# Performance work log

Hardware: AMD Instinct MI355X
Metric: run time of the kernel (lower is better)

The kernel has to match this reference:

```python
import jax, jax.numpy as jnp
import numpy as np

N = 100000      # nodes
E = 1600000     # edges (avg degree 16)
NFEAT = 128
NHID = 128
LRELU_SLOPE = 0.2

def setup_inputs() -> dict:
    key = jax.random.key(0)
    ks = jax.random.split(key, 12)
    s = 1.0 / np.sqrt(NFEAT)
    inp = {}
    inp["x"] = jax.random.normal(ks[0], (N, NFEAT), dtype=jnp.float32)
    inp["edge_row"] = jax.random.randint(ks[1], (E,), 0, N, dtype=jnp.int32)
    inp["edge_col"] = jax.random.randint(ks[2], (E,), 0, N, dtype=jnp.int32)
    inp["edge_val"] = jax.random.uniform(ks[3], (E,), dtype=jnp.float32)
    inp["norm"] = jax.random.uniform(ks[4], (N, 1), dtype=jnp.float32) * 16.0 + 1.0
    # Relation params (bias-free Linears, torch layout y = x @ W.T)
    inp["Wg1"] = jax.random.uniform(ks[5], (NFEAT, NFEAT), minval=-s, maxval=s, dtype=jnp.float32)
    inp["Wg2"] = jax.random.uniform(ks[6], (NFEAT, NFEAT), minval=-s, maxval=s, dtype=jnp.float32)
    inp["Wb1"] = jax.random.uniform(ks[7], (NFEAT, NFEAT), minval=-s, maxval=s, dtype=jnp.float32)
    inp["Wb2"] = jax.random.uniform(ks[8], (NFEAT, NFEAT), minval=-s, maxval=s, dtype=jnp.float32)
    inp["r"] = jax.random.uniform(ks[9], (1, NFEAT), minval=-s, maxval=s, dtype=jnp.float32)
    # GraphConv weight [nfeat, nhid]
    inp["gc_w"] = jax.random.uniform(ks[10], (NFEAT, NHID), minval=-s, maxval=s, dtype=jnp.float32)
    return inp

def _spmm(edge_row, edge_col, edge_val, h):
    # sparse [N,N] @ dense [N,D] via gather + segment-sum
    return jax.ops.segment_sum(edge_val[:, None] * h[edge_col], edge_row, num_segments=N)

def reference(x, edge_row, edge_col, edge_val, norm, Wg1, Wg2, Wb1, Wb2, r, gc_w):
    # neighbor = sp.mm(adj, x)
    neighbor = _spmm(edge_row, edge_col, edge_val, x)
    # Relation (ver=1, ablation=0): FiLM-modulated transE relation vector
    gamma = jax.nn.leaky_relu(x @ Wg1.T + neighbor @ Wg2.T, LRELU_SLOPE) + 1.0
    beta = jax.nn.leaky_relu(x @ Wb1.T + neighbor @ Wb2.T, LRELU_SLOPE)
    m = x + (gamma * r + beta) - neighbor
    # tail branch (head=False, ablation=0): h_s = m @ gc.weight
    h_s = m @ gc_w
    # GraphConv with adj_self = adj + I (no norm inside)
    xw = x @ gc_w
    h_k = _spmm(edge_row, edge_col, edge_val, xw) + xw
    h_k = (h_k + h_s) / (norm + 1.0)
    return (h_k, m)
```

## Files before the change

kernel.cpp:

```cpp
#include <hip/hip_runtime.h>

#define N_NODES 100000
#define NFEAT 128
#define E_EDGES 1600000
#define LRELU_SLOPE 0.2f
#define BM 32
#define NB2 3125
#define SCAP 2048
#define HB_BLOCKS 256
#define HB_PER 6250
#define XB_BLOCKS 3125
#define PK_BLOCKS 320
#define SCAN_P 16

typedef short bf16x8 __attribute__((ext_vector_type(8)));
typedef float f32x4 __attribute__((ext_vector_type(4)));

__device__ __forceinline__ ushort f2bf(float f) {
    union { float f; uint u; } v; v.f = f;
    uint u = v.u;
    return (ushort)((u + 0x7fffu + ((u >> 16) & 1u)) >> 16);
}
__device__ __forceinline__ float bf2f(ushort s) {
    union { uint u; float f; } v; v.u = ((uint)s) << 16;
    return v.f;
}
__device__ __forceinline__ float blo(uint u) {
    union { uint u; float f; } v; v.u = u << 16; return v.f;
}
__device__ __forceinline__ float bhi(uint u) {
    union { uint u; float f; } v; v.u = u & 0xFFFF0000u; return v.f;
}

__global__ __launch_bounds__(256) void mega_prep(
    const int* __restrict__ er, int* __restrict__ ghist,
    const float* __restrict__ x, ushort* __restrict__ xb,
    const float* __restrict__ Wg1, const float* __restrict__ Wg2,
    const float* __restrict__ Wb1, const float* __restrict__ Wb2,
    const float* __restrict__ gcw,
    ushort* __restrict__ W1p, ushort* __restrict__ W2p)
{
    __shared__ int hist[NB2];
    const int bid = blockIdx.x;
    const int tid = threadIdx.x;

    if (bid < HB_BLOCKS) {
        for (int k = tid; k < NB2; k += 256) hist[k] = 0;
        __syncthreads();
        const int e0 = bid * HB_PER;
#pragma unroll 4
        for (int k = tid; k < HB_PER; k += 256)
            atomicAdd(&hist[er[e0 + k] >> 5], 1);
        __syncthreads();
        for (int k = tid; k < NB2; k += 256) ghist[bid * NB2 + k] = hist[k];
    } else if (bid < HB_BLOCKS + XB_BLOCKS) {
        size_t base = ((size_t)(bid - HB_BLOCKS) * 256 + tid) * 16;
        float4 a = *reinterpret_cast<const float4*>(x + base);
        float4 b = *reinterpret_cast<const float4*>(x + base + 4);
        float4 c = *reinterpret_cast<const float4*>(x + base + 8);
        float4 d = *reinterpret_cast<const float4*>(x + base + 12);
        uint4 o1, o2;
        o1.x = (uint)f2bf(a.x) | ((uint)f2bf(a.y) << 16);
        o1.y = (uint)f2bf(a.z) | ((uint)f2bf(a.w) << 16);
        o1.z = (uint)f2bf(b.x) | ((uint)f2bf(b.y) << 16);
        o1.w = (uint)f2bf(b.z) | ((uint)f2bf(b.w) << 16);
        o2.x = (uint)f2bf(c.x) | ((uint)f2bf(c.y) << 16);
        o2.y = (uint)f2bf(c.z) | ((uint)f2bf(c.w) << 16);
        o2.z = (uint)f2bf(d.x) | ((uint)f2bf(d.y) << 16);
        o2.w = (uint)f2bf(d.z) | ((uint)f2bf(d.w) << 16);
        *reinterpret_cast<uint4*>(xb + base) = o1;
        *reinterpret_cast<uint4*>(xb + base + 8) = o2;
    } else {
        int idx = (bid - HB_BLOCKS - XB_BLOCKS) * 256 + tid;
        if (idx < 65536) {
            int jj = idx & 7;
            int lane = (idx >> 3) & 63;
            int tile = idx >> 9;
            int nt = tile & 15, kt = tile >> 4;
            int k = kt * 32 + (lane >> 4) * 8 + jj;
            int j = nt * 16 + (lane & 15);
            float v;
            if (j < 128) v = (k < 128) ? Wg1[j * 128 + k] : Wg2[j * 128 + (k - 128)];
            else { int c = j - 128; v = (k < 128) ? Wb1[c * 128 + k] : Wb2[c * 128 + (k - 128)]; }
            W1p[idx] = f2bf(v);
        } else if (idx < 81920) {
            int i2 = idx - 65536;
            int jj = i2 & 7;
            int lane = (i2 >> 3) & 63;
            int tile = i2 >> 9;
            int nt = tile & 7, kt = tile >> 3;
            int k = kt * 32 + (lane >> 4) * 8 + jj;
            int j = nt * 16 + (lane & 15);
            W2p[i2] = f2bf(gcw[k * 128 + j]);
        }
    }
}

__global__ __launch_bounds__(256) void scan_s(
    const int* __restrict__ ghist, int* __restrict__ S)
{
    int t = blockIdx.x * 256 + threadIdx.x;
    if (t >= SCAN_P * NB2) return;
    int c = t % NB2, p = t / NB2;
    int acc = 0;
#pragma unroll
    for (int r = p * 16; r < p * 16 + 16; r++) acc += ghist[r * NB2 + c];
    S[p * NB2 + c] = acc;
}

__global__ __launch_bounds__(256) void scan_w(
    const int* __restrict__ ghist, const int* __restrict__ S,
    int* __restrict__ gbase, int* __restrict__ cursorB)
{
    int t = blockIdx.x * 256 + threadIdx.x;
    if (t >= SCAN_P * NB2) return;
    int c = t % NB2, p = t / NB2;
    int base = c * SCAP;
    for (int q = 0; q < p; q++) base += S[q * NB2 + c];
#pragma unroll
    for (int r = p * 16; r < p * 16 + 16; r++) {
        gbase[r * NB2 + c] = base;
        base += ghist[r * NB2 + c];
    }
    if (p == SCAN_P - 1) cursorB[c] = base - c * SCAP;
}

__global__ __launch_bounds__(512) void scatter_edges(
    const int* __restrict__ er, const int* __restrict__ ec,
    const float* __restrict__ ev, const int* __restrict__ gbase,
    int2* __restrict__ stg)
{
    __shared__ int cur[NB2];
    const int bid = blockIdx.x;
    const int tid = threadIdx.x;
    for (int k = tid; k < NB2; k += 512) cur[k] = gbase[bid * NB2 + k];
    __syncthreads();
    const int e0 = bid * HB_PER;
#pragma unroll 4
    for (int k = tid; k < HB_PER; k += 512) {
        int e = e0 + k;
        int r = er[e];
        int t = atomicAdd(&cur[r >> 5], 1);
        int2 o;
        o.x = (ec[e] << 13) | (r & 31);
        o.y = __float_as_int(ev[e]);
        stg[t] = o;
    }
}

__global__ __launch_bounds__(512, 8) void fused_all(
    const int* __restrict__ cursorB, const int2* stg,
    const ushort* __restrict__ xb,
    const float* __restrict__ norm, const float* __restrict__ rvec,
    const ushort* __restrict__ W1p, const ushort* __restrict__ W2p,
    float* hk, float* __restrict__ mout)
{
    __shared__ ushort SM[16384];
    __shared__ int h32[32], rs32[32], pd32[32], cur32[32];
    char* asb = (char*)SM;
    char* gbb = (char*)(SM + 8192);
    int2* elist = (int2*)gbb;

    const int tid = threadIdx.x;
    const int lane = tid & 63;
    const int w = tid >> 6;
    const int g = lane >> 4;
    const int s = lane & 15;
    const int b = blockIdx.x;
    const int node0 = b * BM;

    const int2* sb = stg + (size_t)b * SCAP;
    int2 E0 = sb[tid];
    int2 E1 = sb[tid + 512];
    const int cntE = cursorB[b];

    {
        int rr = tid >> 4;
        int cq = tid & 15;
        uint4 v = *reinterpret_cast<const uint4*>(xb + (size_t)(node0 + rr) * 128 + cq * 8);
        *(uint4*)(asb + ((rr * 512 + cq * 16) ^ ((rr & 7) << 4))) = v;
    }

    const bool v0 = tid < cntE, v1 = tid + 512 < cntE;
    if (tid < 32) h32[tid] = 0;
    __syncthreads();
    if (v0) atomicAdd(&h32[E0.x & 31], 1);
    if (v1) atomicAdd(&h32[E1.x & 31], 1);
    __syncthreads();
    if (tid < 64) {
        int pc = 0;
        if (tid < 32) { int h = h32[tid]; pc = (h + 7) & ~7; cur32[tid] = 0; }
        int v = pc;
        for (int off = 1; off < 32; off <<= 1) {
            int t = __shfl_up(v, off, 64);
            if (lane >= off) v += t;
        }
        if (tid < 32) { rs32[tid] = v - pc; pd32[tid] = pc; }
    }
    __syncthreads();
    if (v0) { int rl = E0.x & 31; elist[rs32[rl] + atomicAdd(&cur32[rl], 1)] = E0; }
    if (v1) { int rl = E1.x & 31; elist[rs32[rl] + atomicAdd(&cur32[rl], 1)] = E1; }
    if (tid < 32) {
        int rs = rs32[tid];
        for (int j = h32[tid]; j < pd32[tid]; ++j) elist[rs + j] = make_int2(tid, 0);
    }
    __syncthreads();

    const char* xbase = (const char*)xb + s * 16;
#pragma unroll 1
    for (int i = 0; i < 4; i++) {
        int rr = w * 4 + i;
        const int2* el = elist + rs32[rr];
        int pd = pd32[rr];
        float ac0 = 0.f, ac1 = 0.f, ac2 = 0.f, ac3 = 0.f;
        float ac4 = 0.f, ac5 = 0.f, ac6 = 0.f, ac7 = 0.f;
#pragma unroll 2
        for (int j = 0; j < pd; j += 8) {
            int2 e0 = el[j + g];
            int2 e1 = el[j + 4 + g];
            uint4 q0 = *reinterpret_cast<const uint4*>(xbase + (e0.x >> 5));
            uint4 q1 = *reinterpret_cast<const uint4*>(xbase + (e1.x >> 5));
            float f0 = __int_as_float(e0.y);
            float f1 = __int_as_float(e1.y);
            ac0 += f0 * blo(q0.x); ac1 += f0 * bhi(q0.x);
            ac2 += f0 * blo(q0.y); ac3 += f0 * bhi(q0.y);
            ac4 += f0 * blo(q0.z); ac5 += f0 * bhi(q0.z);
            ac6 += f0 * blo(q0.w); ac7 += f0 * bhi(q0.w);
            ac0 += f1 * blo(q1.x); ac1 += f1 * bhi(q1.x);
            ac2 += f1 * blo(q1.y); ac3 += f1 * bhi(q1.y);
            ac4 += f1 * blo(q1.z); ac5 += f1 * bhi(q1.z);
            ac6 += f1 * blo(q1.w); ac7 += f1 * bhi(q1.w);
        }
        ac0 += __shfl_xor(ac0, 16, 64); ac0 += __shfl_xor(ac0, 32, 64);
        ac1 += __shfl_xor(ac1, 16, 64); ac1 += __shfl_xor(ac1, 32, 64);
        ac2 += __shfl_xor(ac2, 16, 64); ac2 += __shfl_xor(ac2, 32, 64);
        ac3 += __shfl_xor(ac3, 16, 64); ac3 += __shfl_xor(ac3, 32, 64);
        ac4 += __shfl_xor(ac4, 16, 64); ac4 += __shfl_xor(ac4, 32, 64);
        ac5 += __shfl_xor(ac5, 16, 64); ac5 += __shfl_xor(ac5, 32, 64);
        ac6 += __shfl_xor(ac6, 16, 64); ac6 += __shfl_xor(ac6, 32, 64);
        ac7 += __shfl_xor(ac7, 16, 64); ac7 += __shfl_xor(ac7, 32, 64);
        if (g == 0) {
            uint4 o;
            o.x = (uint)f2bf(ac0) | ((uint)f2bf(ac1) << 16);
            o.y = (uint)f2bf(ac2) | ((uint)f2bf(ac3) << 16);
            o.z = (uint)f2bf(ac4) | ((uint)f2bf(ac5) << 16);
            o.w = (uint)f2bf(ac6) | ((uint)f2bf(ac7) << 16);
            *(uint4*)(asb + ((rr * 512 + 256 + s * 16) ^ ((rr & 7) << 4))) = o;
        }
    }

    #define W1L(kt, nl) (*(const bf16x8*)(W1p + ((((kt) * 16 + w * 2 + (nl)) * 64 + lane) << 3)))
    bf16x8 wc0 = W1L(0, 0), wc1 = W1L(0, 1);
    bf16x8 wn0 = W1L(1, 0), wn1 = W1L(1, 1);
    __syncthreads();

    f32x4 acc[2][2];
#pragma unroll
    for (int mt = 0; mt < 2; mt++)
#pragma unroll
        for (int nl = 0; nl < 2; nl++) acc[mt][nl] = (f32x4){0.f, 0.f, 0.f, 0.f};

#pragma unroll
    for (int kt = 0; kt < 8; kt++) {
        bf16x8 wf0, wf1;
        if (kt < 6) { wf0 = W1L(kt + 2, 0); wf1 = W1L(kt + 2, 1); }
        bf16x8 af[2];
#pragma unroll
        for (int mt = 0; mt < 2; mt++) {
            int row = mt * 16 + (lane & 15);
            int off = (row * 512 + kt * 64 + (lane >> 4) * 16) ^ ((row & 7) << 4);
            af[mt] = *(bf16x8*)(asb + off);
        }
#pragma unroll
        for (int mt = 0; mt < 2; mt++) {
            acc[mt][0] = __builtin_amdgcn_mfma_f32_16x16x32_bf16(af[mt], wc0, acc[mt][0], 0, 0, 0);
            acc[mt][1] = __builtin_amdgcn_mfma_f32_16x16x32_bf16(af[mt], wc1, acc[mt][1], 0, 0, 0);
        }
        wc0 = wn0; wc1 = wn1;
        if (kt < 6) { wn0 = wf0; wn1 = wf1; }
    }
    #undef W1L

#pragma unroll
    for (int mt = 0; mt < 2; mt++)
#pragma unroll
        for (int nl = 0; nl < 2; nl++) {
            int j = (w * 2 + nl) * 16 + (lane & 15);
#pragma unroll
            for (int reg = 0; reg < 4; reg++) {
                int row = mt * 16 + (lane >> 4) * 4 + reg;
                int off = (row * 512 + j * 2) ^ ((row & 7) << 4);
                *(ushort*)(gbb + off) = f2bf(acc[mt][nl][reg]);
            }
        }
    __syncthreads();

    {
        int c = tid & 127;
        float rv = rvec[c];
        int rg = tid >> 7;
#pragma unroll 4
        for (int i = 0; i < 8; i++) {
            int row = rg * 8 + i;
            int swz = (row & 7) << 4;
            int bx = (row * 512 + c * 2) ^ swz;
            int bn = (row * 512 + 256 + c * 2) ^ swz;
            float graw = bf2f(*(ushort*)(gbb + bx));
            float braw = bf2f(*(ushort*)(gbb + bn));
            float xv = bf2f(*(ushort*)(asb + bx));
            float nv = bf2f(*(ushort*)(asb + bn));
            float gamma = ((graw > 0.f) ? graw : LRELU_SLOPE * graw) + 1.f;
            float beta = (braw > 0.f) ? braw : LRELU_SLOPE * braw;
            float gb_ = gamma * rv + beta;
            float mv = xv + gb_ - nv;
            float tv = 2.f * xv + gb_;
            mout[(size_t)(node0 + row) * 128 + c] = mv;
            *(ushort*)(asb + bx) = f2bf(tv);
        }
    }

    #define W2L(kt) (*(const bf16x8*)(W2p + ((((kt) * 8 + w) * 64 + lane) << 3)))
    bf16x8 vc = W2L(0);
    bf16x8 vn = W2L(1);
    __syncthreads();

    f32x4 acc2[2];
#pragma unroll
    for (int mt = 0; mt < 2; mt++) acc2[mt] = (f32x4){0.f, 0.f, 0.f, 0.f};

#pragma unroll
    for (int kt = 0; kt < 4; kt++) {
        bf16x8 vf;
        if (kt < 2) vf = W2L(kt + 2);
        bf16x8 af[2];
#pragma unroll
        for (int mt = 0; mt < 2; mt++) {
            int row = mt * 16 + (lane & 15);
            int off = (row * 512 + kt * 64 + (lane >> 4) * 16) ^ ((row & 7) << 4);
            af[mt] = *(bf16x8*)(asb + off);
        }
#pragma unroll
        for (int mt = 0; mt < 2; mt++)
            acc2[mt] = __builtin_amdgcn_mfma_f32_16x16x32_bf16(af[mt], vc, acc2[mt], 0, 0, 0);
        vc = vn;
        if (kt < 2) vn = vf;
    }
    #undef W2L

#pragma unroll
    for (int mt = 0; mt < 2; mt++) {
        int col = w * 16 + (lane & 15);
#pragma unroll
        for (int reg = 0; reg < 4; reg++) {
            int row = mt * 16 + (lane >> 4) * 4 + reg;
            int node = node0 + row;
            float inv = 1.f / (norm[node] + 1.f);
            hk[(size_t)node * 128 + col] = acc2[mt][reg] * inv;
        }
    }
}

extern "C" void kernel_launch(void* const* d_in, const int* in_sizes, int n_in,
                              void* d_out, int out_size, void* d_ws, size_t ws_size,
                              hipStream_t stream)
{
    const float* x    = (const float*)d_in[0];
    const int*   er   = (const int*)d_in[1];
    const int*   ec   = (const int*)d_in[2];
    const float* ev   = (const float*)d_in[3];
    const float* norm = (const float*)d_in[4];
    const float* Wg1  = (const float*)d_in[5];
    const float* Wg2  = (const float*)d_in[6];
    const float* Wb1  = (const float*)d_in[7];
    const float* Wb2  = (const float*)d_in[8];
    const float* r    = (const float*)d_in[9];
    const float* gcw  = (const float*)d_in[10];

    float* out  = (float*)d_out;
    float* hk   = out;
    float* mout = out + (size_t)N_NODES * NFEAT;

    ushort* xb      = (ushort*)d_ws;
    ushort* W1p     = xb + (size_t)N_NODES * NFEAT;
    ushort* W2p     = W1p + 65536;
    int*    cursorB = (int*)(W2p + 16384);
    int*    ghist   = cursorB + NB2;
    int*    gbase   = ghist + HB_BLOCKS * NB2;

    int*  S   = (int*)mout;
    int2* stg = (int2*)hk;

    mega_prep<<<HB_BLOCKS + XB_BLOCKS + PK_BLOCKS, 256, 0, stream>>>(
        er, ghist, x, xb, Wg1, Wg2, Wb1, Wb2, gcw, W1p, W2p);

    scan_s<<<(SCAN_P * NB2 + 255) / 256, 256, 0, stream>>>(ghist, S);

    scan_w<<<(SCAN_P * NB2 + 255) / 256, 256, 0, stream>>>(ghist, S, gbase, cursorB);

    scatter_edges<<<HB_BLOCKS, 512, 0, stream>>>(er, ec, ev, gbase, stg);

    fused_all<<<NB2, 512, 0, stream>>>(
        cursorB, stg, xb, norm, r, W1p, W2p, hk, mout);
}
```

Baseline: 153.2 us.

## Interleave four rows' neighbor gathers per wave and drop weight prefetch registers

The SpMM gather loop now processes all four of a wave's destination rows at once, issuing eight independent bf16 row loads per iteration so more memory requests are in flight. Rows shorter than the longest are masked to a zero weight and a dummy gather from offset 0, which adds some redundant loads. The register-based software prefetch of W1/W2 fragments is removed in favour of direct loads inside the MFMA loops. Launch bounds are relaxed from 8 to 4 waves per SIMD to fit the larger 32-float accumulator set, and edge-list loads are now guarded by the edge count.

Result: no change. 154.8 us (+1.0%).

```diff
diff --git a/kernel.cpp b/kernel.cpp
--- a/kernel.cpp
+++ b/kernel.cpp
@@ -148,7 +148,7 @@
     }
 }
 
-__global__ __launch_bounds__(512, 8) void fused_all(
+__global__ __launch_bounds__(512, 4) void fused_all(
     const int* __restrict__ cursorB, const int2* stg,
     const ushort* __restrict__ xb,
     const float* __restrict__ norm, const float* __restrict__ rvec,
@@ -169,10 +169,12 @@
     const int b = blockIdx.x;
     const int node0 = b * BM;
 
+    const int cntE = cursorB[b];
     const int2* sb = stg + (size_t)b * SCAP;
-    int2 E0 = sb[tid];
-    int2 E1 = sb[tid + 512];
-    const int cntE = cursorB[b];
+    int2 E0, E1;
+    const bool v0 = tid < cntE, v1 = tid + 512 < cntE;
+    if (v0) E0 = sb[tid];
+    if (v1) E1 = sb[tid + 512];
 
     {
         int rr = tid >> 4;
@@ -181,7 +183,6 @@
         *(uint4*)(asb + ((rr * 512 + cq * 16) ^ ((rr & 7) << 4))) = v;
     }
 
-    const bool v0 = tid < cntE, v1 = tid + 512 < cntE;
     if (tid < 32) h32[tid] = 0;
     __syncthreads();
     if (v0) atomicAdd(&h32[E0.x & 31], 1);
@@ -207,63 +208,79 @@
     __syncthreads();
 
     const char* xbase = (const char*)xb + s * 16;
+    const int r0 = w * 4;
+    const int pds0 = pd32[r0 + 0], pds1 = pd32[r0 + 1];
+    const int pds2 = pd32[r0 + 2], pds3 = pd32[r0 + 3];
+    const int2* el0 = elist + rs32[r0 + 0];
+    const int2* el1 = elist + rs32[r0 + 1];
+    const int2* el2 = elist + rs32[r0 + 2];
+    const int2* el3 = elist + rs32[r0 + 3];
+    const int pdm = max(max(pds0, pds1), max(pds2, pds3));
+
+    float acc[4][8];
+#pragma unroll
+    for (int r = 0; r < 4; r++)
+#pragma unroll
+        for (int q = 0; q < 8; q++) acc[r][q] = 0.f;
+
 #pragma unroll 1
-    for (int i = 0; i < 4; i++) {
-        int rr = w * 4 + i;
-        const int2* el = elist + rs32[rr];
-        int pd = pd32[rr];
-        float ac0 = 0.f, ac1 = 0.f, ac2 = 0.f, ac3 = 0.f;
-        float ac4 = 0.f, ac5 = 0.f, ac6 = 0.f, ac7 = 0.f;
-#pragma unroll 2
-        for (int j = 0; j < pd; j += 8) {
+    for (int j = 0; j < pdm; j += 8) {
+        uint4 q0[4], q1[4];
+        float f0[4], f1[4];
+#pragma unroll
+        for (int r = 0; r < 4; r++) {
+            const int2* el = (r == 0) ? el0 : (r == 1) ? el1 : (r == 2) ? el2 : el3;
+            const int pd = (r == 0) ? pds0 : (r == 1) ? pds1 : (r == 2) ? pds2 : pds3;
+            const bool act = j < pd;
             int2 e0 = el[j + g];
             int2 e1 = el[j + 4 + g];
-            uint4 q0 = *reinterpret_cast<const uint4*>(xbase + (e0.x >> 5));
-            uint4 q1 = *reinterpret_cast<const uint4*>(xbase + (e1.x >> 5));
-            float f0 = __int_as_float(e0.y);
-            float f1 = __int_as_float(e1.y);
-            ac0 += f0 * blo(q0.x); ac1 += f0 * bhi(q0.x);
-            ac2 += f0 * blo(q0.y); ac3 += f0 * bhi(q0.y);
-            ac4 += f0 * blo(q0.z); ac5 += f0 * bhi(q0.z);
-            ac6 += f0 * blo(q0.w); ac7 += f0 * bhi(q0.w);
-            ac0 += f1 * blo(q1.x); ac1 += f1 * bhi(q1.x);
-            ac2 += f1 * blo(q1.y); ac3 += f1 * bhi(q1.y);
-            ac4 += f1 * blo(q1.z); ac5 += f1 * bhi(q1.z);
-            ac6 += f1 * blo(q1.w); ac7 += f1 * bhi(q1.w);
-        }
-        ac0 += __shfl_xor(ac0, 16, 64); ac0 += __shfl_xor(ac0, 32, 64);
-        ac1 += __shfl_xor(ac1, 16, 64); ac1 += __shfl_xor(ac1, 32, 64);
-        ac2 += __shfl_xor(ac2, 16, 64); ac2 += __shfl_xor(ac2, 32, 64);
-        ac3 += __shfl_xor(ac3, 16, 64); ac3 += __shfl_xor(ac3, 32, 64);
-        ac4 += __shfl_xor(ac4, 16, 64); ac4 += __shfl_xor(ac4, 32, 64);
-        ac5 += __shfl_xor(ac5, 16, 64); ac5 += __shfl_xor(ac5, 32, 64);
-        ac6 += __shfl_xor(ac6, 16, 64); ac6 += __shfl_xor(ac6, 32, 64);
-        ac7 += __shfl_xor(ac7, 16, 64); ac7 += __shfl_xor(ac7, 32, 64);
+            int o0 = act ? (e0.x >> 5) : 0;
+            int o1 = act ? (e1.x >> 5) : 0;
+            q0[r] = *reinterpret_cast<const uint4*>(xbase + o0);
+            q1[r] = *reinterpret_cast<const uint4*>(xbase + o1);
+            f0[r] = act ? __int_as_float(e0.y) : 0.f;
+            f1[r] = act ? __int_as_float(e1.y) : 0.f;
+        }
+#pragma unroll
+        for (int r = 0; r < 4; r++) {
+            acc[r][0] += f0[r] * blo(q0[r].x); acc[r][1] += f0[r] * bhi(q0[r].x);
+            acc[r][2] += f0[r] * blo(q0[r].y); acc[r][3] += f0[r] * bhi(q0[r].y);
+            acc[r][4] += f0[r] * blo(q0[r].z); acc[r][5] += f0[r] * bhi(q0[r].z);
+            acc[r][6] += f0[r] * blo(q0[r].w); acc[r][7] += f0[r] * bhi(q0[r].w);
+            acc[r][0] += f1[r] * blo(q1[r].x); acc[r][1] += f1[r] * bhi(q1[r].x);
+            acc[r][2] += f1[r] * blo(q1[r].y); acc[r][3] += f1[r] * bhi(q1[r].y);
+            acc[r][4] += f1[r] * blo(q1[r].z); acc[r][5] += f1[r] * bhi(q1[r].z);
+            acc[r][6] += f1[r] * blo(q1[r].w); acc[r][7] += f1[r] * bhi(q1[r].w);
+        }
+    }
+
+#pragma unroll
+    for (int r = 0; r < 4; r++) {
+#pragma unroll
+        for (int q = 0; q < 8; q++) {
+            acc[r][q] += __shfl_xor(acc[r][q], 16, 64);
+            acc[r][q] += __shfl_xor(acc[r][q], 32, 64);
+        }
         if (g == 0) {
+            int rr = r0 + r;
             uint4 o;
-            o.x = (uint)f2bf(ac0) | ((uint)f2bf(ac1) << 16);
-            o.y = (uint)f2bf(ac2) | ((uint)f2bf(ac3) << 16);
-            o.z = (uint)f2bf(ac4) | ((uint)f2bf(ac5) << 16);
-            o.w = (uint)f2bf(ac6) | ((uint)f2bf(ac7) << 16);
+            o.x = (uint)f2bf(acc[r][0]) | ((uint)f2bf(acc[r][1]) << 16);
+            o.y = (uint)f2bf(acc[r][2]) | ((uint)f2bf(acc[r][3]) << 16);
+            o.z = (uint)f2bf(acc[r][4]) | ((uint)f2bf(acc[r][5]) << 16);
+            o.w = (uint)f2bf(acc[r][6]) | ((uint)f2bf(acc[r][7]) << 16);
             *(uint4*)(asb + ((rr * 512 + 256 + s * 16) ^ ((rr & 7) << 4))) = o;
         }
     }
-
-    #define W1L(kt, nl) (*(const bf16x8*)(W1p + ((((kt) * 16 + w * 2 + (nl)) * 64 + lane) << 3)))
-    bf16x8 wc0 = W1L(0, 0), wc1 = W1L(0, 1);
-    bf16x8 wn0 = W1L(1, 0), wn1 = W1L(1, 1);
-    __syncthreads();
-
-    f32x4 acc[2][2];
+    __syncthreads();
+
+    f32x4 acc1[2][2];
 #pragma unroll
     for (int mt = 0; mt < 2; mt++)
 #pragma unroll
-        for (int nl = 0; nl < 2; nl++) acc[mt][nl] = (f32x4){0.f, 0.f, 0.f, 0.f};
+        for (int nl = 0; nl < 2; nl++) acc1[mt][nl] = (f32x4){0.f, 0.f, 0.f, 0.f};
 
 #pragma unroll
     for (int kt = 0; kt < 8; kt++) {
-        bf16x8 wf0, wf1;
-        if (kt < 6) { wf0 = W1L(kt + 2, 0); wf1 = W1L(kt + 2, 1); }
         bf16x8 af[2];
 #pragma unroll
         for (int mt = 0; mt < 2; mt++) {
@@ -272,14 +289,14 @@
             af[mt] = *(bf16x8*)(asb + off);
         }
 #pragma unroll
-        for (int mt = 0; mt < 2; mt++) {
-            acc[mt][0] = __builtin_amdgcn_mfma_f32_16x16x32_bf16(af[mt], wc0, acc[mt][0], 0, 0, 0);
-            acc[mt][1] = __builtin_amdgcn_mfma_f32_16x16x32_bf16(af[mt], wc1, acc[mt][1], 0, 0, 0);
-        }
-        wc0 = wn0; wc1 = wn1;
-        if (kt < 6) { wn0 = wf0; wn1 = wf1; }
-    }
-    #undef W1L
+        for (int nl = 0; nl < 2; nl++) {
+            int nt = w * 2 + nl;
+            bf16x8 bfg = *(const bf16x8*)(W1p + (((kt * 16 + nt) * 64 + lane) << 3));
+#pragma unroll
+            for (int mt = 0; mt < 2; mt++)
+                acc1[mt][nl] = __builtin_amdgcn_mfma_f32_16x16x32_bf16(af[mt], bfg, acc1[mt][nl], 0, 0, 0);
+        }
+    }
 
 #pragma unroll
     for (int mt = 0; mt < 2; mt++)
@@ -290,7 +307,7 @@
             for (int reg = 0; reg < 4; reg++) {
                 int row = mt * 16 + (lane >> 4) * 4 + reg;
                 int off = (row * 512 + j * 2) ^ ((row & 7) << 4);
-                *(ushort*)(gbb + off) = f2bf(acc[mt][nl][reg]);
+                *(ushort*)(gbb + off) = f2bf(acc1[mt][nl][reg]);
             }
         }
     __syncthreads();
@@ -318,10 +335,6 @@
             *(ushort*)(asb + bx) = f2bf(tv);
         }
     }
-
-    #define W2L(kt) (*(const bf16x8*)(W2p + ((((kt) * 8 + w) * 64 + lane) << 3)))
-    bf16x8 vc = W2L(0);
-    bf16x8 vn = W2L(1);
     __syncthreads();
 
     f32x4 acc2[2];
@@ -330,8 +343,6 @@
 
 #pragma unroll
     for (int kt = 0; kt < 4; kt++) {
-        bf16x8 vf;
-        if (kt < 2) vf = W2L(kt + 2);
         bf16x8 af[2];
 #pragma unroll
         for (int mt = 0; mt < 2; mt++) {
@@ -339,13 +350,11 @@
             int off = (row * 512 + kt * 64 + (lane >> 4) * 16) ^ ((row & 7) << 4);
             af[mt] = *(bf16x8*)(asb + off);
         }
+        bf16x8 bfg = *(const bf16x8*)(W2p + (((kt * 8 + w) * 64 + lane) << 3));
 #pragma unroll
         for (int mt = 0; mt < 2; mt++)
-            acc2[mt] = __builtin_amdgcn_mfma_f32_16x16x32_bf16(af[mt], vc, acc2[mt], 0, 0, 0);
-        vc = vn;
-        if (kt < 2) vn = vf;
-    }
-    #undef W2L
+            acc2[mt] = __builtin_amdgcn_mfma_f32_16x16x32_bf16(af[mt], bfg, acc2[mt], 0, 0, 0);
+    }
 
 #pragma unroll
     for (int mt = 0; mt < 2; mt++) {
```

## Balance per-warp row gather with dynamic work counter and simplify weight loads

Applied to the files above, without the earlier changes.

Replaces the static assignment of four rows per wave in the sparse gather phase with a shared atomic row counter, so waves pull rows dynamically to even out load across rows with varying degree. Staged edge loads are now predicated on the edge count to skip reading unused staging slots. The software-prefetched weight fragments for both MFMA stages are replaced by direct per-iteration global loads, which lowers register pressure but exposes weight-load latency inside the MFMA loops.

After: 148.6 us. 3.0% less time.

```diff
diff --git a/kernel.cpp b/kernel.cpp
--- a/kernel.cpp
+++ b/kernel.cpp
@@ -157,6 +157,7 @@
 {
     __shared__ ushort SM[16384];
     __shared__ int h32[32], rs32[32], pd32[32], cur32[32];
+    __shared__ int rowctr;
     char* asb = (char*)SM;
     char* gbb = (char*)(SM + 8192);
     int2* elist = (int2*)gbb;
@@ -169,10 +170,12 @@
     const int b = blockIdx.x;
     const int node0 = b * BM;
 
+    const int cntE = cursorB[b];
     const int2* sb = stg + (size_t)b * SCAP;
-    int2 E0 = sb[tid];
-    int2 E1 = sb[tid + 512];
-    const int cntE = cursorB[b];
+    int2 E0, E1;
+    const bool v0 = tid < cntE, v1 = tid + 512 < cntE;
+    if (v0) E0 = sb[tid];
+    if (v1) E1 = sb[tid + 512];
 
     {
         int rr = tid >> 4;
@@ -181,8 +184,8 @@
         *(uint4*)(asb + ((rr * 512 + cq * 16) ^ ((rr & 7) << 4))) = v;
     }
 
-    const bool v0 = tid < cntE, v1 = tid + 512 < cntE;
     if (tid < 32) h32[tid] = 0;
+    if (tid == 32) rowctr = 0;
     __syncthreads();
     if (v0) atomicAdd(&h32[E0.x & 31], 1);
     if (v1) atomicAdd(&h32[E1.x & 31], 1);
@@ -207,9 +210,11 @@
     __syncthreads();
 
     const char* xbase = (const char*)xb + s * 16;
-#pragma unroll 1
-    for (int i = 0; i < 4; i++) {
-        int rr = w * 4 + i;
+    for (;;) {
+        int rr;
+        if (lane == 0) rr = atomicAdd(&rowctr, 1);
+        rr = __shfl(rr, 0, 64);
+        if (rr >= 32) break;
         const int2* el = elist + rs32[rr];
         int pd = pd32[rr];
         float ac0 = 0.f, ac1 = 0.f, ac2 = 0.f, ac3 = 0.f;
@@ -248,10 +253,6 @@
             *(uint4*)(asb + ((rr * 512 + 256 + s * 16) ^ ((rr & 7) << 4))) = o;
         }
     }
-
-    #define W1L(kt, nl) (*(const bf16x8*)(W1p + ((((kt) * 16 + w * 2 + (nl)) * 64 + lane) << 3)))
-    bf16x8 wc0 = W1L(0, 0), wc1 = W1L(0, 1);
-    bf16x8 wn0 = W1L(1, 0), wn1 = W1L(1, 1);
     __syncthreads();
 
     f32x4 acc[2][2];
@@ -262,8 +263,6 @@
 
 #pragma unroll
     for (int kt = 0; kt < 8; kt++) {
-        bf16x8 wf0, wf1;
-        if (kt < 6) { wf0 = W1L(kt + 2, 0); wf1 = W1L(kt + 2, 1); }
         bf16x8 af[2];
 #pragma unroll
         for (int mt = 0; mt < 2; mt++) {
@@ -272,14 +271,14 @@
             af[mt] = *(bf16x8*)(asb + off);
         }
 #pragma unroll
-        for (int mt = 0; mt < 2; mt++) {
-            acc[mt][0] = __builtin_amdgcn_mfma_f32_16x16x32_bf16(af[mt], wc0, acc[mt][0], 0, 0, 0);
-            acc[mt][1] = __builtin_amdgcn_mfma_f32_16x16x32_bf16(af[mt], wc1, acc[mt][1], 0, 0, 0);
-        }
-        wc0 = wn0; wc1 = wn1;
-        if (kt < 6) { wn0 = wf0; wn1 = wf1; }
-    }
-    #undef W1L
+        for (int nl = 0; nl < 2; nl++) {
+            int nt = w * 2 + nl;
+            bf16x8 bfg = *(const bf16x8*)(W1p + (((kt * 16 + nt) * 64 + lane) << 3));
+#pragma unroll
+            for (int mt = 0; mt < 2; mt++)
+                acc[mt][nl] = __builtin_amdgcn_mfma_f32_16x16x32_bf16(af[mt], bfg, acc[mt][nl], 0, 0, 0);
+        }
+    }
 
 #pragma unroll
     for (int mt = 0; mt < 2; mt++)
@@ -318,10 +317,6 @@
             *(ushort*)(asb + bx) = f2bf(tv);
         }
     }
-
-    #define W2L(kt) (*(const bf16x8*)(W2p + ((((kt) * 8 + w) * 64 + lane) << 3)))
-    bf16x8 vc = W2L(0);
-    bf16x8 vn = W2L(1);
     __syncthreads();
 
     f32x4 acc2[2];
@@ -330,8 +325,6 @@
 
 #pragma unroll
     for (int kt = 0; kt < 4; kt++) {
-        bf16x8 vf;
-        if (kt < 2) vf = W2L(kt + 2);
         bf16x8 af[2];
 #pragma unroll
         for (int mt = 0; mt < 2; mt++) {
@@ -339,13 +332,11 @@
             int off = (row * 512 + kt * 64 + (lane >> 4) * 16) ^ ((row & 7) << 4);
             af[mt] = *(bf16x8*)(asb + off);
         }
+        bf16x8 bfg = *(const bf16x8*)(W2p + (((kt * 8 + w) * 64 + lane) << 3));
 #pragma unroll
         for (int mt = 0; mt < 2; mt++)
-            acc2[mt] = __builtin_amdgcn_mfma_f32_16x16x32_bf16(af[mt], vc, acc2[mt], 0, 0, 0);
-        vc = vn;
-        if (kt < 2) vn = vf;
-    }
-    #undef W2L
+            acc2[mt] = __builtin_amdgcn_mfma_f32_16x16x32_bf16(af[mt], bfg, acc2[mt], 0, 0, 0);
+    }
 
 #pragma unroll
     for (int mt = 0; mt < 2; mt++) {
```
